# Performance work log

Measured on AMD Instinct MI355X. Metric: run time of the kernel, lower is better.

The kernel has to match this reference:

```python
import jax, jax.numpy as jnp
import numpy as np

B, S, D = 4, 2048, 1024
NB_HEAD, SIZE_PER_HEAD = 16, 64  # output_dim = 1024


def setup_inputs() -> dict:
    key = jax.random.key(0)
    ks = jax.random.split(key, 6)
    out_dim = NB_HEAD * SIZE_PER_HEAD
    return {
        "q_seq": jax.random.normal(ks[0], (B, S, D), dtype=jnp.float32),
        "k_seq": jax.random.normal(ks[1], (B, S, D), dtype=jnp.float32),
        "v_seq": jax.random.normal(ks[2], (B, S, D), dtype=jnp.float32),
        "WQ": jax.random.normal(ks[3], (D, out_dim), dtype=jnp.float32) * (1.0 / np.sqrt(D)),
        "WK": jax.random.normal(ks[4], (D, out_dim), dtype=jnp.float32) * (1.0 / np.sqrt(D)),
        "WV": jax.random.normal(ks[5], (D, out_dim), dtype=jnp.float32) * (1.0 / np.sqrt(D)),
    }


def reference(q_seq, k_seq, v_seq, WQ, WK, WV):
    h, dh = NB_HEAD, SIZE_PER_HEAD
    b, sq, _ = q_seq.shape
    sk = k_seq.shape[1]
    # QKV projections, then split heads: [b, s, h*dh] -> [b, h, s, dh]
    Q = (q_seq @ WQ).reshape(b, sq, h, dh).transpose(0, 2, 1, 3)
    Kp = (k_seq @ WK).reshape(b, sk, h, dh).transpose(0, 2, 1, 3)
    V = (v_seq @ WV).reshape(b, sk, h, dh).transpose(0, 2, 1, 3)
    scale = 1.0 / jnp.sqrt(jnp.asarray(dh, dtype=Q.dtype))
    # scores [b, h, q, k]; V_len is None so no additive mask is applied
    A = jnp.einsum("bhqd,bhkd->bhqk", Q, Kp) * scale
    A = jax.nn.softmax(A, axis=-1)
    O = jnp.einsum("bhqk,bhkd->bhqd", A, V)
    # merge heads back: [b, q, h*dh]; Q_len is None so no mul-mask
    return O.transpose(0, 2, 1, 3).reshape(b, sq, h * dh)
```

## Files before the change

kernel.cpp:

```cpp
#include <hip/hip_runtime.h>
#include <hip/hip_bf16.h>
#include <stdint.h>

#define B_ 4
#define S_ 2048
#define D_ 1024
#define H_ 16
#define DH_ 64
#define BH_ 64
#define M_ 8192

typedef __bf16 bf16;
typedef __attribute__((ext_vector_type(4))) __bf16 bf16x4;
typedef __attribute__((ext_vector_type(8))) __bf16 bf16x8;
typedef __attribute__((ext_vector_type(4))) float f32x4;
typedef __attribute__((ext_vector_type(8))) float f32x8;

#define EXP2F(x) __builtin_amdgcn_exp2f(x)

__device__ inline void gload16(const void* g, void* l) {
  __builtin_amdgcn_global_load_lds((const __attribute__((address_space(1))) void*)g,
                                   (__attribute__((address_space(3))) void*)l, 16, 0, 0);
}

__global__ __launch_bounds__(256) void k_conv(const float* __restrict__ q,
    const float* __restrict__ k, const float* __restrict__ v, bf16* __restrict__ o) {
  int z = blockIdx.y;
  const float* s = z == 0 ? q : (z == 1 ? k : v);
  bf16* d = o + (size_t)z * ((size_t)M_ * D_);
  int n8 = M_ * D_ / 8;
  for (int i = blockIdx.x * 256 + threadIdx.x; i < n8; i += gridDim.x * 256) {
    f32x8 f = ((const f32x8*)s)[i];
    bf16x8 b;
#pragma unroll
    for (int j = 0; j < 8; j++) b[j] = (bf16)f[j];
    ((bf16x8*)d)[i] = b;
  }
}

__global__ __launch_bounds__(256) void k_wt(const float* __restrict__ wq,
    const float* __restrict__ wk, const float* __restrict__ wv, bf16* __restrict__ o) {
  __shared__ float t[32][33];
  int z = blockIdx.z;
  const float* w = z == 0 ? wq : (z == 1 ? wk : wv);
  bf16* d = o + (size_t)z * D_ * D_;
  int bn = blockIdx.x * 32;
  int bk = blockIdx.y * 32;
  int tx = threadIdx.x & 31, ty = threadIdx.x >> 5;
#pragma unroll
  for (int j = 0; j < 32; j += 8) t[ty + j][tx] = w[(size_t)(bk + ty + j) * D_ + bn + tx];
  __syncthreads();
#pragma unroll
  for (int j = 0; j < 32; j += 8)
    d[(size_t)(bn + ty + j) * D_ + bk + tx] = (bf16)t[tx][ty + j];
}

__global__ __launch_bounds__(256) void k_proj(const bf16* __restrict__ X,
    const bf16* __restrict__ WT, bf16* __restrict__ Qo, bf16* __restrict__ Ko,
    bf16* __restrict__ VTo) {
  __shared__ bf16 lds[16384];
  int z = blockIdx.z;
  const char* Ab = (const char*)(X + (size_t)z * M_ * D_);
  const char* Bb = (const char*)(WT + (size_t)z * D_ * D_);
  int m0 = blockIdx.x * 128, n0 = blockIdx.y * 128;
  int tid = threadIdx.x, lane = tid & 63, w = tid >> 6;
  int wr = w >> 1, wc = w & 1, fr = lane & 15, fg = lane >> 4;
  f32x4 acc[4][4];
#pragma unroll
  for (int a = 0; a < 4; a++)
#pragma unroll
    for (int b = 0; b < 4; b++) acc[a][b] = (f32x4){0.f, 0.f, 0.f, 0.f};

  for (int k0 = 0; k0 < D_; k0 += 64) {
#pragma unroll
    for (int it = 0; it < 8; ++it) {
      int ow = (w + 4 * it) * 1024;
      int o = ow + lane * 16;
      const char* src;
      if (o < 16384) {
        int row = o >> 7;
        int db = (o & 127) ^ ((row & 7) << 4);
        src = Ab + (size_t)(m0 + row) * 2048 + k0 * 2 + db;
      } else {
        int lo = o - 16384, row = lo >> 7;
        int db = (lo & 127) ^ ((row & 7) << 4);
        src = Bb + (size_t)(n0 + row) * 2048 + k0 * 2 + db;
      }
      gload16(src, (char*)lds + ow);
    }
    __syncthreads();
#pragma unroll
    for (int c = 0; c < 2; c++) {
      bf16x8 af[4], bfr[4];
#pragma unroll
      for (int mi = 0; mi < 4; mi++) {
        int row = wr * 64 + mi * 16 + fr;
        af[mi] = *(const bf16x8*)&lds[row * 64 + ((fg * 8 + 32 * c) ^ ((row & 7) << 3))];
      }
#pragma unroll
      for (int ni = 0; ni < 4; ni++) {
        int row = wc * 64 + ni * 16 + fr;
        bfr[ni] = *(const bf16x8*)&lds[8192 + row * 64 + ((fg * 8 + 32 * c) ^ ((row & 7) << 3))];
      }
#pragma unroll
      for (int mi = 0; mi < 4; mi++)
#pragma unroll
        for (int ni = 0; ni < 4; ni++)
          acc[mi][ni] = __builtin_amdgcn_mfma_f32_16x16x32_bf16(af[mi], bfr[ni],
                                                                acc[mi][ni], 0, 0, 0);
    }
    __syncthreads();
  }
  if (z == 2) {
#pragma unroll
    for (int mi = 0; mi < 4; mi++) {
      int row = m0 + wr * 64 + mi * 16 + 4 * fg;
      int bI = row >> 11, s = row & 2047;
      int blk = s >> 6, kk = s & 63;
      int slot = (kk & 0x23) | ((kk & 0x0C) << 1) | ((kk & 0x10) >> 2);
#pragma unroll
      for (int ni = 0; ni < 4; ni++) {
        int col = n0 + wc * 64 + ni * 16 + fr;
        int h = col >> 6, d = col & 63;
        bf16x4 vv = (bf16x4){(bf16)acc[mi][ni][0], (bf16)acc[mi][ni][1],
                             (bf16)acc[mi][ni][2], (bf16)acc[mi][ni][3]};
        *(bf16x4*)&VTo[((size_t)(bI * H_ + h) * DH_ + d) * S_ + blk * 64 + slot] = vv;
      }
    }
  } else {
    bf16* O = z == 0 ? Qo : Ko;
    float sc = (z == 0) ? 0.18033688011112042f : 1.0f;
#pragma unroll
    for (int mi = 0; mi < 4; mi++)
#pragma unroll
      for (int r = 0; r < 4; r++) {
        int row = m0 + wr * 64 + mi * 16 + 4 * fg + r;
        int b = row >> 11, s = row & 2047;
#pragma unroll
        for (int ni = 0; ni < 4; ni++) {
          int col = n0 + wc * 64 + ni * 16 + fr;
          int h = col >> 6, d = col & 63;
          O[((size_t)(b * H_ + h) * S_ + s) * DH_ + d] = (bf16)(acc[mi][ni][r] * sc);
        }
      }
  }
}

__global__ __launch_bounds__(512, 8) void k_attn(const bf16* __restrict__ Q,
    const bf16* __restrict__ Kt, const bf16* __restrict__ VT, float* __restrict__ out) {
  __shared__ bf16 kv[16384];
  int g = blockIdx.x;
  int wg = (g & 7) * 128 + (g >> 3);
  int qt = wg & 15, bh = wg >> 4;
  int b = bh >> 4, h = bh & 15;
  int tid = threadIdx.x, lane = tid & 63, w = tid >> 6;
  int fr = lane & 15, fg = lane >> 4;
  const char* Kb = (const char*)(Kt + (size_t)bh * S_ * DH_);
  const char* Vb = (const char*)(VT + (size_t)bh * DH_ * S_);
  int q0 = qt * 128 + w * 16;

  int o0 = tid * 16;
  int r0 = o0 >> 7, b0 = (o0 & 127) ^ ((r0 & 7) << 4);
  const char* kp = Kb + r0 * 128 + b0;
  const char* vp = Vb + r0 * 4096 + b0;
  char* lb = (char*)kv;
  int w1024 = w * 1024;

  const int swz = (fr & 7) << 3;
  const bf16* kb0 = &kv[fr * 64 + ((fg * 8) ^ swz)];
  const bf16* kb1 = &kv[fr * 64 + ((fg * 8 + 32) ^ swz)];
  const bf16* vb0 = kb0 + 4096;
  const bf16* vb1 = kb1 + 4096;

  bf16x8 qf[2];
#pragma unroll
  for (int c = 0; c < 2; c++)
    qf[c] = *(const bf16x8*)(Q + ((size_t)bh * S_ + q0 + fr) * DH_ + fg * 8 + 32 * c);
  float m_ = -1e30f;
  f32x4 o_[4];
#pragma unroll
  for (int ds = 0; ds < 4; ds++) o_[ds] = (f32x4){0.f, 0.f, 0.f, 0.f};
  f32x4 ol = (f32x4){0.f, 0.f, 0.f, 0.f};
  bf16x8 vones;
#pragma unroll
  for (int j = 0; j < 8; j++) vones[j] = (bf16)1.0f;

  gload16(kp, lb + w1024);
  gload16(vp, lb + 8192 + w1024);
  kp += 8192; vp += 128;

#pragma unroll 2
  for (int kt = 0; kt < 32; ++kt) {
    __syncthreads();
    if (kt + 1 < 32) {
      const int nb = ((kt + 1) & 1) << 14;
      gload16(kp, lb + nb + w1024);
      gload16(vp, lb + nb + 8192 + w1024);
      kp += 8192; vp += 128;
    }
    const int cb = (kt & 1) << 13;
    f32x4 st[4];
    __builtin_amdgcn_s_setprio(1);
#pragma unroll
    for (int ks = 0; ks < 4; ks++) {
      bf16x8 kf0 = *(const bf16x8*)(kb0 + cb + ks * 1024);
      bf16x8 kf1 = *(const bf16x8*)(kb1 + cb + ks * 1024);
      f32x4 a = (f32x4){0.f, 0.f, 0.f, 0.f};
      a = __builtin_amdgcn_mfma_f32_16x16x32_bf16(kf0, qf[0], a, 0, 0, 0);
      a = __builtin_amdgcn_mfma_f32_16x16x32_bf16(kf1, qf[1], a, 0, 0, 0);
      st[ks] = a;
    }
    __builtin_amdgcn_s_setprio(0);
    float ma = fmaxf(fmaxf(st[0][0], st[0][1]), st[0][2]);
    float mb = fmaxf(fmaxf(st[0][3], st[1][0]), st[1][1]);
    float mc = fmaxf(fmaxf(st[1][2], st[1][3]), st[2][0]);
    float md = fmaxf(fmaxf(st[2][1], st[2][2]), st[2][3]);
    float me = fmaxf(fmaxf(st[3][0], st[3][1]), st[3][2]);
    float mx = fmaxf(fmaxf(fmaxf(ma, mb), mc), fmaxf(fmaxf(md, me), st[3][3]));
    mx = fmaxf(mx, __shfl_xor(mx, 16));
    mx = fmaxf(mx, __shfl_xor(mx, 32));
    if (!__all(mx - m_ <= 7.0f)) {
      float mnew = fmaxf(m_, mx);
      float sf = EXP2F(m_ - mnew);
      m_ = mnew;
      float s0 = __shfl(sf, 4 * fg + 0);
      float s1 = __shfl(sf, 4 * fg + 1);
      float s2 = __shfl(sf, 4 * fg + 2);
      float s3 = __shfl(sf, 4 * fg + 3);
#pragma unroll
      for (int ds = 0; ds < 4; ds++) {
        o_[ds][0] *= s0; o_[ds][1] *= s1;
        o_[ds][2] *= s2; o_[ds][3] *= s3;
      }
      ol[0] *= s0; ol[1] *= s1; ol[2] *= s2; ol[3] *= s3;
    }
#pragma unroll
    for (int ks = 0; ks < 4; ks++)
#pragma unroll
      for (int r = 0; r < 4; r++) st[ks][r] = EXP2F(st[ks][r] - m_);
    bf16x8 pa[2];
    pa[0] = (bf16x8){(bf16)st[0][0], (bf16)st[0][1], (bf16)st[0][2], (bf16)st[0][3],
                     (bf16)st[1][0], (bf16)st[1][1], (bf16)st[1][2], (bf16)st[1][3]};
    pa[1] = (bf16x8){(bf16)st[2][0], (bf16)st[2][1], (bf16)st[2][2], (bf16)st[2][3],
                     (bf16)st[3][0], (bf16)st[3][1], (bf16)st[3][2], (bf16)st[3][3]};
    __builtin_amdgcn_s_setprio(1);
    ol = __builtin_amdgcn_mfma_f32_16x16x32_bf16(pa[0], vones, ol, 0, 0, 0);
    ol = __builtin_amdgcn_mfma_f32_16x16x32_bf16(pa[1], vones, ol, 0, 0, 0);
#pragma unroll
    for (int c = 0; c < 2; c++) {
      const bf16* vbc = c ? vb1 : vb0;
#pragma unroll
      for (int ds = 0; ds < 4; ds++) {
        bf16x8 vf = *(const bf16x8*)(vbc + cb + ds * 1024);
        o_[ds] = __builtin_amdgcn_mfma_f32_16x16x32_bf16(pa[c], vf, o_[ds], 0, 0, 0);
      }
    }
    __builtin_amdgcn_s_setprio(0);
  }
#pragma unroll
  for (int r = 0; r < 4; r++) {
    float inv = 1.0f / ol[r];
    int s = q0 + 4 * fg + r;
#pragma unroll
    for (int ds = 0; ds < 4; ds++) {
      int col = h * DH_ + ds * 16 + fr;
      out[((size_t)b * S_ + s) * D_ + col] = o_[ds][r] * inv;
    }
  }
}

extern "C" void kernel_launch(void* const* d_in, const int* in_sizes, int n_in,
                              void* d_out, int out_size, void* d_ws, size_t ws_size,
                              hipStream_t stream) {
  (void)in_sizes; (void)n_in; (void)out_size; (void)ws_size;
  const float* q  = (const float*)d_in[0];
  const float* k  = (const float*)d_in[1];
  const float* v  = (const float*)d_in[2];
  const float* wq = (const float*)d_in[3];
  const float* wk = (const float*)d_in[4];
  const float* wv = (const float*)d_in[5];
  float* out = (float*)d_out;
  char* ws = (char*)d_ws;
  size_t off = 0;
  bf16* xb = (bf16*)(ws + off); off += (size_t)3 * M_ * D_ * 2;
  bf16* wt = (bf16*)(ws + off); off += (size_t)3 * D_ * D_ * 2;
  bf16* Qw = (bf16*)(ws + off); off += (size_t)BH_ * S_ * DH_ * 2;
  bf16* Kw = (bf16*)(ws + off); off += (size_t)BH_ * S_ * DH_ * 2;
  bf16* Vt = (bf16*)(ws + off); off += (size_t)BH_ * S_ * DH_ * 2;

  k_conv<<<dim3(1024, 3), 256, 0, stream>>>(q, k, v, xb);
  k_wt  <<<dim3(32, 32, 3), 256, 0, stream>>>(wq, wk, wv, wt);
  k_proj<<<dim3(64, 8, 3), 256, 0, stream>>>(xb, wt, Qw, Kw, Vt);
  k_attn<<<dim3(1024), 512, 0, stream>>>(Qw, Kw, Vt, out);
}
```

Baseline: 184.8 us.

## Process two 16-row query tiles per wave in attention to reuse K/V fragments

Each wave in the attention kernel now handles 32 query rows (two 16-row MFMA tiles) instead of 16, so every workgroup covers 256 queries and the grid halves to 512 blocks. K and V fragments loaded from LDS are reused across both query tiles, halving the LDS reads and global K/V streaming per query. In exchange, register use roughly doubles for accumulators and scores, so launch bounds drop to 4 blocks per CU. With 512 blocks the grid may also fill the 256 CUs less evenly.

```diff
diff --git a/kernel.cpp b/kernel.cpp
--- a/kernel.cpp
+++ b/kernel.cpp
@@ -146,18 +146,18 @@
   }
 }
 
-__global__ __launch_bounds__(512, 8) void k_attn(const bf16* __restrict__ Q,
+__global__ __launch_bounds__(512, 4) void k_attn(const bf16* __restrict__ Q,
     const bf16* __restrict__ Kt, const bf16* __restrict__ VT, float* __restrict__ out) {
   __shared__ bf16 kv[16384];
   int g = blockIdx.x;
-  int wg = (g & 7) * 128 + (g >> 3);
-  int qt = wg & 15, bh = wg >> 4;
+  int wg = (g & 7) * 64 + (g >> 3);
+  int qt = wg & 7, bh = wg >> 3;
   int b = bh >> 4, h = bh & 15;
   int tid = threadIdx.x, lane = tid & 63, w = tid >> 6;
   int fr = lane & 15, fg = lane >> 4;
   const char* Kb = (const char*)(Kt + (size_t)bh * S_ * DH_);
   const char* Vb = (const char*)(VT + (size_t)bh * DH_ * S_);
-  int q0 = qt * 128 + w * 16;
+  int q0 = qt * 256 + w * 32;
 
   int o0 = tid * 16;
   int r0 = o0 >> 7, b0 = (o0 & 127) ^ ((r0 & 7) << 4);
@@ -172,15 +172,19 @@
   const bf16* vb0 = kb0 + 4096;
   const bf16* vb1 = kb1 + 4096;
 
-  bf16x8 qf[2];
-#pragma unroll
-  for (int c = 0; c < 2; c++)
-    qf[c] = *(const bf16x8*)(Q + ((size_t)bh * S_ + q0 + fr) * DH_ + fg * 8 + 32 * c);
-  float m_ = -1e30f;
-  f32x4 o_[4];
-#pragma unroll
-  for (int ds = 0; ds < 4; ds++) o_[ds] = (f32x4){0.f, 0.f, 0.f, 0.f};
-  f32x4 ol = (f32x4){0.f, 0.f, 0.f, 0.f};
+  bf16x8 qf[2][2];
+#pragma unroll
+  for (int mi = 0; mi < 2; mi++)
+#pragma unroll
+    for (int c = 0; c < 2; c++)
+      qf[mi][c] = *(const bf16x8*)(Q + ((size_t)bh * S_ + q0 + mi * 16 + fr) * DH_ + fg * 8 + 32 * c);
+  float m_[2] = {-1e30f, -1e30f};
+  f32x4 o_[2][4];
+#pragma unroll
+  for (int mi = 0; mi < 2; mi++)
+#pragma unroll
+    for (int ds = 0; ds < 4; ds++) o_[mi][ds] = (f32x4){0.f, 0.f, 0.f, 0.f};
+  f32x4 ol[2] = {(f32x4){0.f, 0.f, 0.f, 0.f}, (f32x4){0.f, 0.f, 0.f, 0.f}};
   bf16x8 vones;
 #pragma unroll
   for (int j = 0; j < 8; j++) vones[j] = (bf16)1.0f;
@@ -199,74 +203,88 @@
       kp += 8192; vp += 128;
     }
     const int cb = (kt & 1) << 13;
-    f32x4 st[4];
+    f32x4 st[2][4];
     __builtin_amdgcn_s_setprio(1);
 #pragma unroll
     for (int ks = 0; ks < 4; ks++) {
       bf16x8 kf0 = *(const bf16x8*)(kb0 + cb + ks * 1024);
       bf16x8 kf1 = *(const bf16x8*)(kb1 + cb + ks * 1024);
-      f32x4 a = (f32x4){0.f, 0.f, 0.f, 0.f};
-      a = __builtin_amdgcn_mfma_f32_16x16x32_bf16(kf0, qf[0], a, 0, 0, 0);
-      a = __builtin_amdgcn_mfma_f32_16x16x32_bf16(kf1, qf[1], a, 0, 0, 0);
-      st[ks] = a;
+#pragma unroll
+      for (int mi = 0; mi < 2; mi++) {
+        f32x4 a = (f32x4){0.f, 0.f, 0.f, 0.f};
+        a = __builtin_amdgcn_mfma_f32_16x16x32_bf16(kf0, qf[mi][0], a, 0, 0, 0);
+        a = __builtin_amdgcn_mfma_f32_16x16x32_bf16(kf1, qf[mi][1], a, 0, 0, 0);
+        st[mi][ks] = a;
+      }
     }
     __builtin_amdgcn_s_setprio(0);
-    float ma = fmaxf(fmaxf(st[0][0], st[0][1]), st[0][2]);
-    float mb = fmaxf(fmaxf(st[0][3], st[1][0]), st[1][1]);
-    float mc = fmaxf(fmaxf(st[1][2], st[1][3]), st[2][0]);
-    float md = fmaxf(fmaxf(st[2][1], st[2][2]), st[2][3]);
-    float me = fmaxf(fmaxf(st[3][0], st[3][1]), st[3][2]);
-    float mx = fmaxf(fmaxf(fmaxf(ma, mb), mc), fmaxf(fmaxf(md, me), st[3][3]));
-    mx = fmaxf(mx, __shfl_xor(mx, 16));
-    mx = fmaxf(mx, __shfl_xor(mx, 32));
-    if (!__all(mx - m_ <= 7.0f)) {
-      float mnew = fmaxf(m_, mx);
-      float sf = EXP2F(m_ - mnew);
-      m_ = mnew;
-      float s0 = __shfl(sf, 4 * fg + 0);
-      float s1 = __shfl(sf, 4 * fg + 1);
-      float s2 = __shfl(sf, 4 * fg + 2);
-      float s3 = __shfl(sf, 4 * fg + 3);
-#pragma unroll
-      for (int ds = 0; ds < 4; ds++) {
-        o_[ds][0] *= s0; o_[ds][1] *= s1;
-        o_[ds][2] *= s2; o_[ds][3] *= s3;
-      }
-      ol[0] *= s0; ol[1] *= s1; ol[2] *= s2; ol[3] *= s3;
-    }
-#pragma unroll
-    for (int ks = 0; ks < 4; ks++)
-#pragma unroll
-      for (int r = 0; r < 4; r++) st[ks][r] = EXP2F(st[ks][r] - m_);
-    bf16x8 pa[2];
-    pa[0] = (bf16x8){(bf16)st[0][0], (bf16)st[0][1], (bf16)st[0][2], (bf16)st[0][3],
-                     (bf16)st[1][0], (bf16)st[1][1], (bf16)st[1][2], (bf16)st[1][3]};
-    pa[1] = (bf16x8){(bf16)st[2][0], (bf16)st[2][1], (bf16)st[2][2], (bf16)st[2][3],
-                     (bf16)st[3][0], (bf16)st[3][1], (bf16)st[3][2], (bf16)st[3][3]};
+    bf16x8 pa[2][2];
+#pragma unroll
+    for (int mi = 0; mi < 2; mi++) {
+      float ma = fmaxf(fmaxf(st[mi][0][0], st[mi][0][1]), st[mi][0][2]);
+      float mb = fmaxf(fmaxf(st[mi][0][3], st[mi][1][0]), st[mi][1][1]);
+      float mc = fmaxf(fmaxf(st[mi][1][2], st[mi][1][3]), st[mi][2][0]);
+      float md = fmaxf(fmaxf(st[mi][2][1], st[mi][2][2]), st[mi][2][3]);
+      float me = fmaxf(fmaxf(st[mi][3][0], st[mi][3][1]), st[mi][3][2]);
+      float mx = fmaxf(fmaxf(fmaxf(ma, mb), mc), fmaxf(fmaxf(md, me), st[mi][3][3]));
+      mx = fmaxf(mx, __shfl_xor(mx, 16));
+      mx = fmaxf(mx, __shfl_xor(mx, 32));
+      if (!__all(mx - m_[mi] <= 7.0f)) {
+        float mnew = fmaxf(m_[mi], mx);
+        float sf = EXP2F(m_[mi] - mnew);
+        m_[mi] = mnew;
+        float s0 = __shfl(sf, 4 * fg + 0);
+        float s1 = __shfl(sf, 4 * fg + 1);
+        float s2 = __shfl(sf, 4 * fg + 2);
+        float s3 = __shfl(sf, 4 * fg + 3);
+#pragma unroll
+        for (int ds = 0; ds < 4; ds++) {
+          o_[mi][ds][0] *= s0; o_[mi][ds][1] *= s1;
+          o_[mi][ds][2] *= s2; o_[mi][ds][3] *= s3;
+        }
+        ol[mi][0] *= s0; ol[mi][1] *= s1; ol[mi][2] *= s2; ol[mi][3] *= s3;
+      }
+#pragma unroll
+      for (int ks = 0; ks < 4; ks++)
+#pragma unroll
+        for (int r = 0; r < 4; r++) st[mi][ks][r] = EXP2F(st[mi][ks][r] - m_[mi]);
+      pa[mi][0] = (bf16x8){(bf16)st[mi][0][0], (bf16)st[mi][0][1], (bf16)st[mi][0][2],
+                           (bf16)st[mi][0][3], (bf16)st[mi][1][0], (bf16)st[mi][1][1],
+                           (bf16)st[mi][1][2], (bf16)st[mi][1][3]};
+      pa[mi][1] = (bf16x8){(bf16)st[mi][2][0], (bf16)st[mi][2][1], (bf16)st[mi][2][2],
+                           (bf16)st[mi][2][3], (bf16)st[mi][3][0], (bf16)st[mi][3][1],
+                           (bf16)st[mi][3][2], (bf16)st[mi][3][3]};
+    }
     __builtin_amdgcn_s_setprio(1);
-    ol = __builtin_amdgcn_mfma_f32_16x16x32_bf16(pa[0], vones, ol, 0, 0, 0);
-    ol = __builtin_amdgcn_mfma_f32_16x16x32_bf16(pa[1], vones, ol, 0, 0, 0);
+#pragma unroll
+    for (int mi = 0; mi < 2; mi++) {
+      ol[mi] = __builtin_amdgcn_mfma_f32_16x16x32_bf16(pa[mi][0], vones, ol[mi], 0, 0, 0);
+      ol[mi] = __builtin_amdgcn_mfma_f32_16x16x32_bf16(pa[mi][1], vones, ol[mi], 0, 0, 0);
+    }
 #pragma unroll
     for (int c = 0; c < 2; c++) {
       const bf16* vbc = c ? vb1 : vb0;
 #pragma unroll
       for (int ds = 0; ds < 4; ds++) {
         bf16x8 vf = *(const bf16x8*)(vbc + cb + ds * 1024);
-        o_[ds] = __builtin_amdgcn_mfma_f32_16x16x32_bf16(pa[c], vf, o_[ds], 0, 0, 0);
+        o_[0][ds] = __builtin_amdgcn_mfma_f32_16x16x32_bf16(pa[0][c], vf, o_[0][ds], 0, 0, 0);
+        o_[1][ds] = __builtin_amdgcn_mfma_f32_16x16x32_bf16(pa[1][c], vf, o_[1][ds], 0, 0, 0);
       }
     }
     __builtin_amdgcn_s_setprio(0);
   }
 #pragma unroll
-  for (int r = 0; r < 4; r++) {
-    float inv = 1.0f / ol[r];
-    int s = q0 + 4 * fg + r;
-#pragma unroll
-    for (int ds = 0; ds < 4; ds++) {
-      int col = h * DH_ + ds * 16 + fr;
-      out[((size_t)b * S_ + s) * D_ + col] = o_[ds][r] * inv;
-    }
-  }
+  for (int mi = 0; mi < 2; mi++)
+#pragma unroll
+    for (int r = 0; r < 4; r++) {
+      float inv = 1.0f / ol[mi][r];
+      int s = q0 + mi * 16 + 4 * fg + r;
+#pragma unroll
+      for (int ds = 0; ds < 4; ds++) {
+        int col = h * DH_ + ds * 16 + fr;
+        out[((size_t)b * S_ + s) * D_ + col] = o_[mi][ds][r] * inv;
+      }
+    }
 }
 
 extern "C" void kernel_launch(void* const* d_in, const int* in_sizes, int n_in,
@@ -291,5 +309,5 @@
   k_conv<<<dim3(1024, 3), 256, 0, stream>>>(q, k, v, xb);
   k_wt  <<<dim3(32, 32, 3), 256, 0, stream>>>(wq, wk, wv, wt);
   k_proj<<<dim3(64, 8, 3), 256, 0, stream>>>(xb, wt, Qw, Kw, Vt);
-  k_attn<<<dim3(1024), 512, 0, stream>>>(Qw, Kw, Vt, out);
-}
+  k_attn<<<dim3(512), 512, 0, stream>>>(Qw, Kw, Vt, out);
+}
```

After: 171.3 us. 1.08x faster.
